# Kernel tuning notes

Measured on AMD Instinct MI355X. Metric: run time of the kernel, lower is better.

Reference implementation:

```python
import jax, jax.numpy as jnp
import numpy as np

N_NODES = 50000


def gcn_conv(x, src, dst, W, b, n_nodes):
    """PyG GCNConv: self-loops + symmetric normalization D^-1/2 (A+I) D^-1/2 X W + b."""
    loop = jnp.arange(n_nodes, dtype=src.dtype)
    s = jnp.concatenate([src, loop])
    d = jnp.concatenate([dst, loop])
    deg = jax.ops.segment_sum(jnp.ones_like(d, dtype=x.dtype), d, num_segments=n_nodes)
    dinv = jnp.where(deg > 0, jax.lax.rsqrt(deg), 0.0)
    norm = dinv[s] * dinv[d]  # (E+N,)
    h = x @ W  # (N, out)
    msg = h[s] * norm[:, None]
    return jax.ops.segment_sum(msg, d, num_segments=n_nodes) + b


def setup_inputs() -> dict:
    key = jax.random.key(0)
    ks = jax.random.split(key, 16)
    N, S, D = N_NODES, 20, 128
    E = 1_600_000
    PH, PO, GH, GO = 64, 128, 128, 32

    def lin(k, fan_in, fan_out):
        bound = 1.0 / np.sqrt(fan_in)
        kw, kb = jax.random.split(k)
        W = jax.random.uniform(kw, (fan_in, fan_out), jnp.float32, -bound, bound)
        b = jax.random.uniform(kb, (fan_out,), jnp.float32, -bound, bound)
        return W, b

    W_embed, b_embed = lin(ks[0], D, PH)
    W_attn, b_attn = lin(ks[1], PH, 1)
    W_out, b_out = lin(ks[2], PH, PO)
    W1, b1 = lin(ks[3], PO, GH)
    W2, b2 = lin(ks[4], GH, GO)
    Wm1, bm1 = lin(ks[5], GO, 64)
    Wm2, bm2 = lin(ks[6], 64, 1)

    return {
        "set_features": jax.random.normal(ks[7], (N, S, D), jnp.float32),
        "set_mask": jnp.ones((N, S), jnp.int32),
        "edge_index": jax.random.randint(ks[8], (2, E), 0, N, jnp.int32),
        "query_idx": jax.random.randint(ks[9], (4096,), 0, N, jnp.int32),
        "W_embed": W_embed, "b_embed": b_embed,
        "W_attn": W_attn, "b_attn": b_attn,
        "W_out": W_out, "b_out": b_out,
        "W1": W1, "b1": b1, "W2": W2, "b2": b2,
        "Wm1": Wm1, "bm1": bm1, "Wm2": Wm2, "bm2": bm2,
    }


def reference(set_features, set_mask, edge_index, query_idx,
              W_embed, b_embed, W_attn, b_attn, W_out, b_out,
              W1, b1, W2, b2, Wm1, bm1, Wm2, bm2):
    n_nodes = set_features.shape[0]
    # Attention pooling over each node's set: (N, S, D) -> (N, PO)
    z = jax.nn.relu(set_features @ W_embed + b_embed)          # (N, S, PH)
    scores = (z @ W_attn)[..., 0] + b_attn[0]                  # (N, S)
    scores = jnp.where(set_mask == 0, -jnp.inf, scores)
    attn = jax.nn.softmax(scores, axis=1)                      # (N, S)
    pooled = jnp.einsum('nsh,ns->nh', z, attn) @ W_out + b_out  # (N, PO)

    src, dst = edge_index[0], edge_index[1]
    x = jax.nn.relu(gcn_conv(pooled, src, dst, W1, b1, n_nodes))
    x = jax.nn.relu(gcn_conv(x, src, dst, W2, b2, n_nodes))

    q = x[query_idx]                                            # (B, GO)
    logits = (jax.nn.relu(q @ Wm1 + bm1) @ Wm2 + bm2)[..., 0]   # (B,)
    return logits
```

## Files before the change

### kernel.cpp

```cpp
#include <hip/hip_runtime.h>
#include <math.h>

#define RFL(x) __builtin_amdgcn_readfirstlane(x)
#define RL(x, l) __int_as_float(__builtin_amdgcn_readlane(__float_as_int(x), (l)))

typedef __attribute__((ext_vector_type(8))) short bf16x8;
typedef __attribute__((ext_vector_type(4))) float f32x4;

__device__ inline unsigned short bf16_rne(float f) {
  unsigned u = __float_as_uint(f);
  u += 0x7FFFu + ((u >> 16) & 1u);
  return (unsigned short)(u >> 16);
}


__global__ __launch_bounds__(256) void k_zero(int* p, int n) {
  int t = blockIdx.x * 256 + threadIdx.x;
  if (t < n) p[t] = 0;
}

__global__ __launch_bounds__(256) void k_count(const int* __restrict__ dst, int* cnt, int E) {
  int stride = gridDim.x * blockDim.x;
  for (int e = blockIdx.x * blockDim.x + threadIdx.x; e < E; e += stride)
    atomicAdd(&cnt[dst[e]], 1);
}


__global__ __launch_bounds__(256) void k_scan1(const int* __restrict__ cnt, int* __restrict__ row,
                                               int* __restrict__ partial, int N) {
  __shared__ int sm[256];
  int t = threadIdx.x, g = blockIdx.x * 256 + t;
  int v = (g < N) ? cnt[g] : 0;
  sm[t] = v;
  __syncthreads();
#pragma unroll
  for (int off = 1; off < 256; off <<= 1) {
    int x = 0;
    if (t >= off) x = sm[t - off];
    __syncthreads();
    if (t >= off) sm[t] += x;
    __syncthreads();
  }
  if (g < N) row[g] = sm[t] - v;
  if (t == 255) partial[blockIdx.x] = sm[255];
}

__global__ __launch_bounds__(256) void k_scan2(int* __restrict__ partial, int P) {
  __shared__ int sm[256];
  int t = threadIdx.x;
  int carry = 0;
  for (int base = 0; base < P; base += 256) {
    int idx = base + t;
    int v = (idx < P) ? partial[idx] : 0;
    sm[t] = v;
    __syncthreads();
#pragma unroll
    for (int off = 1; off < 256; off <<= 1) {
      int x = 0;
      if (t >= off) x = sm[t - off];
      __syncthreads();
      if (t >= off) sm[t] += x;
      __syncthreads();
    }
    if (idx < P) partial[idx] = carry + sm[t] - v;
    int tot = sm[255];
    __syncthreads();
    carry += tot;
  }
}

__global__ __launch_bounds__(256) void k_scan3(int* __restrict__ row, const int* __restrict__ partial,
                                               int* __restrict__ cursor, const int* __restrict__ cnt,
                                               float* __restrict__ dinv, int N) {
  int g = blockIdx.x * 256 + threadIdx.x;
  if (g < N) {
    int v = row[g] + partial[blockIdx.x];
    row[g] = v;
    cursor[g] = v;
    dinv[g] = rsqrtf((float)cnt[g] + 1.0f);
  }
}


__global__ __launch_bounds__(256) void k_edge_fill(const int* __restrict__ src, const int* __restrict__ dst,
                                                   int* __restrict__ cursor, int* __restrict__ esrc, int E) {
  int stride = gridDim.x * blockDim.x;
  for (int e = blockIdx.x * blockDim.x + threadIdx.x; e < E; e += stride) {
    int s = src[e], d = dst[e];
    int pos = atomicAdd(&cursor[d], 1);
    esrc[pos] = s;
  }
}


__global__ __launch_bounds__(256) void k_wc(const float* __restrict__ Wout, const float* __restrict__ bout,
                                            const float* __restrict__ W1, float* __restrict__ Wc,
                                            float* __restrict__ bc) {
  int t = blockIdx.x * 256 + threadIdx.x;
  if (t >= 65 * 128) return;
  int h = t >> 7, o = t & 127;
  const float* row = (h < 64) ? (Wout + h * 128) : bout;
  float a = 0.f;
  for (int d = 0; d < 128; ++d) a += row[d] * W1[d * 128 + o];
  if (h < 64) Wc[h * 128 + o] = a;
  else bc[o] = a;
}


__global__ __launch_bounds__(256, 3) void k_pool(const float* __restrict__ X, const int* __restrict__ mask,
                                                 const float* __restrict__ WE, const float* __restrict__ bE,
                                                 const float* __restrict__ WA, const float* __restrict__ bA,
                                                 const float* __restrict__ dinv, float* __restrict__ pzp, int N) {
  __shared__ __align__(16) unsigned short Xh[80][136];
  __shared__ __align__(16) unsigned short Xl[80][136];
  __shared__ float scorep[80][4];
  __shared__ float sco[80];
  __shared__ float wgtA[80];
  float* zt = (float*)&Xh[0][0];

  const int t = threadIdx.x;
  const int lane = t & 63;
  const int wv = t >> 6;
  const int cb = wv * 16;
  const int l16 = lane & 15;
  const int lg = lane >> 4;

  const long long totRows = (long long)N * 20;
  const int numTiles = (N + 3) / 4;

  const int r0 = t >> 5;
  const int kq4 = (t & 31) * 4;

  bf16x8 bh[4], bl[4];
#pragma unroll
  for (int kk = 0; kk < 4; ++kk) {
    union { bf16x8 v; unsigned short s[8]; } uh, ul;
#pragma unroll
    for (int i = 0; i < 8; ++i) {
      int k = kk * 32 + lg * 8 + i;
      float w = WE[k * 64 + cb + l16];
      unsigned short h = bf16_rne(w);
      uh.s[i] = h;
      ul.s[i] = bf16_rne(w - __uint_as_float((unsigned)h << 16));
    }
    bh[kk] = uh.v;
    bl[kk] = ul.v;
  }
  const float bEv = bE[cb + l16];
  const float WAv = WA[cb + l16];
  const float bAv = bA[0];
  const float NEG = -3.0e38f;

  int tile = blockIdx.x;
  if (tile >= numTiles) return;

  float4 xv[10];
#pragma unroll
  for (int q = 0; q < 10; ++q) {
    long long rr = (long long)tile * 80 + r0 + q * 8;
    if (rr >= totRows) rr = totRows - 1;
    xv[q] = *(const float4*)(X + rr * 128 + kq4);
  }
  int mkcur = 1;
  {
    long long mi = (long long)tile * 80 + t;
    if (t < 80) mkcur = (mi < totRows) ? mask[mi] : 0;
  }

  while (true) {
#pragma unroll
    for (int q = 0; q < 10; ++q) {
      const int r = r0 + q * 8;
      const float4 v = xv[q];
      unsigned short h0 = bf16_rne(v.x), h1 = bf16_rne(v.y), h2 = bf16_rne(v.z), h3 = bf16_rne(v.w);
      float f0 = __uint_as_float((unsigned)h0 << 16);
      float f1 = __uint_as_float((unsigned)h1 << 16);
      float f2 = __uint_as_float((unsigned)h2 << 16);
      float f3 = __uint_as_float((unsigned)h3 << 16);
      *(ushort4*)&Xh[r][kq4] = make_ushort4(h0, h1, h2, h3);
      *(ushort4*)&Xl[r][kq4] = make_ushort4(bf16_rne(v.x - f0), bf16_rne(v.y - f1),
                                            bf16_rne(v.z - f2), bf16_rne(v.w - f3));
    }
    __syncthreads();

    const int nextTile = tile + gridDim.x;
    const bool hasNext = nextTile < numTiles;
    float4 xn[10];
    int mknext = 1;
    {
      const long long nb = (long long)(hasNext ? nextTile : tile) * 80;
#pragma unroll
      for (int q = 0; q < 10; ++q) {
        long long rr = nb + r0 + q * 8;
        if (rr >= totRows) rr = totRows - 1;
        xn[q] = *(const float4*)(X + rr * 128 + kq4);
      }
      long long mi = nb + t;
      if (t < 80) mknext = (mi < totRows) ? mask[mi] : 0;
    }

    f32x4 acc[5];
#pragma unroll
    for (int rt = 0; rt < 5; ++rt) acc[rt] = (f32x4){0.f, 0.f, 0.f, 0.f};
#pragma unroll
    for (int rt = 0; rt < 5; ++rt) {
      const int rl = rt * 16 + l16;
#pragma unroll
      for (int kk = 0; kk < 4; ++kk) {
        const int ko = kk * 32 + lg * 8;
        bf16x8 ah = *(const bf16x8*)&Xh[rl][ko];
        bf16x8 al = *(const bf16x8*)&Xl[rl][ko];
        acc[rt] = __builtin_amdgcn_mfma_f32_16x16x32_bf16(ah, bh[kk], acc[rt], 0, 0, 0);
        acc[rt] = __builtin_amdgcn_mfma_f32_16x16x32_bf16(ah, bl[kk], acc[rt], 0, 0, 0);
        acc[rt] = __builtin_amdgcn_mfma_f32_16x16x32_bf16(al, bh[kk], acc[rt], 0, 0, 0);
      }
    }

#pragma unroll
    for (int rt = 0; rt < 5; ++rt) {
#pragma unroll
      for (int j = 0; j < 4; ++j) {
        float z = fmaxf(acc[rt][j] + bEv, 0.f);
        acc[rt][j] = z;
        float v = z * WAv;
        v += __shfl_xor(v, 1, 64);
        v += __shfl_xor(v, 2, 64);
        v += __shfl_xor(v, 4, 64);
        v += __shfl_xor(v, 8, 64);
        if (l16 == 0) scorep[rt * 16 + lg * 4 + j][wv] = v;
      }
    }
    __syncthreads();

#pragma unroll
    for (int rt = 0; rt < 5; ++rt) {
#pragma unroll
      for (int j = 0; j < 4; ++j) {
        int row = rt * 16 + lg * 4 + j;
        zt[row * 68 + cb + l16] = acc[rt][j];
      }
    }
    if (t < 80) {
      float4 sp = *(const float4*)scorep[t];
      float sc = sp.x + sp.y + sp.z + sp.w + bAv;
      if (mkcur == 0) sc = NEG;
      sco[t] = sc;
    }
    __syncthreads();

    if (t < 80) {
      const int base = (t / 20) * 20;
      float mx = NEG;
#pragma unroll
      for (int i = 0; i < 20; ++i) mx = fmaxf(mx, sco[base + i]);
      float den = 0.f;
#pragma unroll
      for (int i = 0; i < 20; ++i) den += __expf(sco[base + i] - mx);
      wgtA[t] = __expf(sco[t] - mx) / den;
    }
    __syncthreads();

    {
      int n = t >> 6, col = t & 63;
      long long node = (long long)tile * 4 + n;
      if (node < N) {
        float s = 0.f;
#pragma unroll
        for (int i = 0; i < 20; ++i) s += zt[(n * 20 + i) * 68 + col] * wgtA[n * 20 + i];
        pzp[node * 64 + col] = s * dinv[node];
      }
    }

    if (!hasNext) break;
    __syncthreads();
#pragma unroll
    for (int q = 0; q < 10; ++q) xv[q] = xn[q];
    mkcur = mknext;
    tile = nextTile;
  }
}


__global__ __launch_bounds__(256) void k_gather1(const int* __restrict__ row, const int* __restrict__ cnt,
                                                 const int* __restrict__ esrc, const float* __restrict__ pzp,
                                                 const float* __restrict__ dinv, float* __restrict__ y,
                                                 float* __restrict__ gout, int N) {
  const int lane = threadIdx.x & 63;
  const int node = RFL(blockIdx.x * 4 + (threadIdx.x >> 6));
  if (node >= N) return;
  const int q = lane >> 4, f4 = lane & 15;
  const int rs = RFL(row[node]);
  const int ne = RFL(cnt[node]);
  const float di = dinv[node];
  const float4* __restrict__ hv = (const float4*)pzp;
  float a0 = 0.f, a1 = 0.f, a2 = 0.f, a3 = 0.f, ds = 0.f;
  int j = 0;
  for (; j + 16 <= ne; j += 16) {
    const int b = rs + j + q * 4;
    int s[4];
#pragma unroll
    for (int u = 0; u < 4; ++u) s[u] = esrc[b + u];
    float4 v[4];
#pragma unroll
    for (int u = 0; u < 4; ++u) v[u] = hv[(size_t)s[u] * 16 + f4];
#pragma unroll
    for (int u = 0; u < 4; ++u) {
      a0 += v[u].x; a1 += v[u].y; a2 += v[u].z; a3 += v[u].w;
      ds += dinv[s[u]];
    }
  }
  if (j < ne) {
    const int b = j + q * 4;
    int s[4];
    float m[4];
#pragma unroll
    for (int u = 0; u < 4; ++u) {
      int idx = b + u;
      int c = (idx < ne) ? idx : (ne - 1);
      s[u] = esrc[rs + c];
      m[u] = (idx < ne) ? 1.f : 0.f;
    }
    float4 v[4];
#pragma unroll
    for (int u = 0; u < 4; ++u) v[u] = hv[(size_t)s[u] * 16 + f4];
#pragma unroll
    for (int u = 0; u < 4; ++u) {
      a0 += v[u].x * m[u]; a1 += v[u].y * m[u]; a2 += v[u].z * m[u]; a3 += v[u].w * m[u];
      ds += dinv[s[u]] * m[u];
    }
  }
  a0 += __shfl_xor(a0, 16, 64); a0 += __shfl_xor(a0, 32, 64);
  a1 += __shfl_xor(a1, 16, 64); a1 += __shfl_xor(a1, 32, 64);
  a2 += __shfl_xor(a2, 16, 64); a2 += __shfl_xor(a2, 32, 64);
  a3 += __shfl_xor(a3, 16, 64); a3 += __shfl_xor(a3, 32, 64);
  ds += __shfl_xor(ds, 16, 64); ds += __shfl_xor(ds, 32, 64);
  if (lane < 16) {
    float4 sv = hv[(size_t)node * 16 + f4];
    float4 o;
    o.x = (a0 + sv.x * di) * di;
    o.y = (a1 + sv.y * di) * di;
    o.z = (a2 + sv.z * di) * di;
    o.w = (a3 + sv.w * di) * di;
    ((float4*)y)[(size_t)node * 16 + f4] = o;
    if (f4 == 0) gout[node] = di * (ds + di * di);
  }
}


__global__ __launch_bounds__(256, 2) void k_gemm1(const float* __restrict__ y, const float* __restrict__ gin,
                                                  const float* __restrict__ Wc, const float* __restrict__ bc,
                                                  float* __restrict__ x1, int N) {
  const int lane = threadIdx.x & 63;
  float w0[64], w1[64];
#pragma unroll
  for (int d = 0; d < 64; ++d) {
    w0[d] = Wc[d * 128 + lane];
    w1[d] = Wc[d * 128 + 64 + lane];
  }
  const float b0 = bc[lane], b1v = bc[64 + lane];
  const int nw = (gridDim.x * blockDim.x) >> 6;
  const int w_id = (blockIdx.x * blockDim.x + threadIdx.x) >> 6;
  for (int r = w_id; r < N; r += nw) {
    const float xv = y[(size_t)r * 64 + lane];
    const float gr = gin[r];
    const int xi = __float_as_int(xv);
    float p0 = 0.f, p1 = 0.f, p2 = 0.f, p3 = 0.f;
#pragma unroll
    for (int d0 = 0; d0 < 64; d0 += 2) {
      float a0 = RL((float&)xi, d0);
      float a1 = RL((float&)xi, d0 + 1);
      p0 += a0 * w0[d0];
      p1 += a0 * w1[d0];
      p2 += a1 * w0[d0 + 1];
      p3 += a1 * w1[d0 + 1];
    }
    size_t o = (size_t)r * 128 + lane;
    x1[o] = p0 + p2 + gr * b0;
    x1[o + 64] = p1 + p3 + gr * b1v;
  }
}


__global__ __launch_bounds__(256, 2) void k_gemm2(const float* __restrict__ x1, const float* __restrict__ b1,
                                                  const float* __restrict__ W2, const float* __restrict__ dinv,
                                                  float* __restrict__ h2p, int N) {
  const int lane = threadIdx.x & 63;
  const int col = lane & 31;
  float w[128];
#pragma unroll
  for (int d = 0; d < 128; ++d) w[d] = W2[d * 32 + col];
  const float bb0 = b1[lane], bb1 = b1[64 + lane];
  const int nw = (gridDim.x * blockDim.x) >> 6;
  const int w_id = (blockIdx.x * blockDim.x + threadIdx.x) >> 6;
  for (int r = w_id; r < N; r += nw) {
    float rx0 = fmaxf(x1[(size_t)r * 128 + lane] + bb0, 0.f);
    float rx1 = fmaxf(x1[(size_t)r * 128 + 64 + lane] + bb1, 0.f);
    const int xi0 = __float_as_int(rx0), xi1 = __float_as_int(rx1);
    float p0 = 0.f, p1 = 0.f, p2 = 0.f, p3 = 0.f;
#pragma unroll
    for (int d0 = 0; d0 < 64; d0 += 2) {
      float a0 = RL((float&)xi0, d0);
      float a1 = RL((float&)xi0, d0 + 1);
      float c0 = RL((float&)xi1, d0);
      float c1 = RL((float&)xi1, d0 + 1);
      p0 += a0 * w[d0];
      p1 += a1 * w[d0 + 1];
      p2 += c0 * w[64 + d0];
      p3 += c1 * w[64 + d0 + 1];
    }
    if (lane < 32) {
      float di = dinv[r];
      h2p[(size_t)r * 32 + col] = ((p0 + p1) + (p2 + p3)) * di;
    }
  }
}


__global__ __launch_bounds__(256) void k_gmlp(const int* __restrict__ qidx, const int* __restrict__ row,
                                              const int* __restrict__ cnt, const int* __restrict__ esrc,
                                              const float* __restrict__ h2p, const float* __restrict__ dinv,
                                              const float* __restrict__ b2, const float* __restrict__ Wm1,
                                              const float* __restrict__ bm1, const float* __restrict__ Wm2,
                                              const float* __restrict__ bm2, float* __restrict__ out, int B) {
  __shared__ float qs[4][32];
  const int lane = threadIdx.x & 63;
  const int wv = threadIdx.x >> 6;
  const int w = blockIdx.x * 4 + wv;
  const int wc = (w < B) ? w : (B - 1);
  const int node = RFL(qidx[wc]);

  const int q = lane >> 3, f4 = lane & 7;
  const int rs = RFL(row[node]);
  const int ne = RFL(cnt[node]);
  const float di = dinv[node];
  const float4* __restrict__ hv = (const float4*)h2p;
  float a0 = 0.f, a1 = 0.f, a2 = 0.f, a3 = 0.f;
  int j = 0;
  for (; j + 32 <= ne; j += 32) {
    const int b = rs + j + q * 4;
    int s[4];
#pragma unroll
    for (int u = 0; u < 4; ++u) s[u] = esrc[b + u];
    float4 v[4];
#pragma unroll
    for (int u = 0; u < 4; ++u) v[u] = hv[(size_t)s[u] * 8 + f4];
#pragma unroll
    for (int u = 0; u < 4; ++u) {
      a0 += v[u].x; a1 += v[u].y; a2 += v[u].z; a3 += v[u].w;
    }
  }
  if (j < ne) {
    const int b = j + q * 4;
    int s[4];
    float m[4];
#pragma unroll
    for (int u = 0; u < 4; ++u) {
      int idx = b + u;
      int c = (idx < ne) ? idx : (ne - 1);
      s[u] = esrc[rs + c];
      m[u] = (idx < ne) ? 1.f : 0.f;
    }
    float4 v[4];
#pragma unroll
    for (int u = 0; u < 4; ++u) v[u] = hv[(size_t)s[u] * 8 + f4];
#pragma unroll
    for (int u = 0; u < 4; ++u) {
      a0 += v[u].x * m[u]; a1 += v[u].y * m[u]; a2 += v[u].z * m[u]; a3 += v[u].w * m[u];
    }
  }
#pragma unroll
  for (int off = 8; off <= 32; off <<= 1) {
    a0 += __shfl_xor(a0, off, 64);
    a1 += __shfl_xor(a1, off, 64);
    a2 += __shfl_xor(a2, off, 64);
    a3 += __shfl_xor(a3, off, 64);
  }
  if (q == 0) {
    float4 sv = hv[(size_t)node * 8 + f4];
    qs[wv][f4 * 4 + 0] = fmaxf((a0 + sv.x * di) * di + b2[f4 * 4 + 0], 0.f);
    qs[wv][f4 * 4 + 1] = fmaxf((a1 + sv.y * di) * di + b2[f4 * 4 + 1], 0.f);
    qs[wv][f4 * 4 + 2] = fmaxf((a2 + sv.z * di) * di + b2[f4 * 4 + 2], 0.f);
    qs[wv][f4 * 4 + 3] = fmaxf((a3 + sv.w * di) * di + b2[f4 * 4 + 3], 0.f);
  }
  __syncthreads();

  float h = bm1[lane];
#pragma unroll
  for (int k = 0; k < 32; ++k) h += qs[wv][k] * Wm1[k * 64 + lane];
  float r = fmaxf(h, 0.f) * Wm2[lane];
#pragma unroll
  for (int off = 1; off < 64; off <<= 1) r += __shfl_xor(r, off, 64);
  if (lane == 0 && w < B) out[w] = r + bm2[0];
}


extern "C" void kernel_launch(void* const* d_in, const int* in_sizes, int n_in,
                              void* d_out, int out_size, void* d_ws, size_t ws_size,
                              hipStream_t stream) {
  const float* X    = (const float*)d_in[0];
  const int*   mask = (const int*)d_in[1];
  const int*   ei   = (const int*)d_in[2];
  const int*   qidx = (const int*)d_in[3];
  const float* WE   = (const float*)d_in[4];
  const float* bE   = (const float*)d_in[5];
  const float* WA   = (const float*)d_in[6];
  const float* bA   = (const float*)d_in[7];
  const float* Wout = (const float*)d_in[8];
  const float* bout = (const float*)d_in[9];
  const float* W1   = (const float*)d_in[10];
  const float* b1   = (const float*)d_in[11];
  const float* W2   = (const float*)d_in[12];
  const float* b2   = (const float*)d_in[13];
  const float* Wm1  = (const float*)d_in[14];
  const float* bm1  = (const float*)d_in[15];
  const float* Wm2  = (const float*)d_in[16];
  const float* bm2  = (const float*)d_in[17];

  const int N = in_sizes[1] / 20;
  const int E = in_sizes[2] / 2;
  const int B = in_sizes[3];
  const int* src  = ei;
  const int* dstp = ei + E;

  const size_t Na = ((size_t)N + 63) & ~(size_t)63;
  const size_t Ea = ((size_t)E + 63) & ~(size_t)63;
  const int P = (N + 255) / 256;
  const size_t Pa = ((size_t)P + 63) & ~(size_t)63;

  float* ws      = (float*)d_ws;
  float* dinv    = ws;
  int*   cnt     = (int*)(dinv + Na);
  int*   rowp    = cnt + Na;
  int*   cursor  = rowp + Na;
  int*   partial = cursor + Na;
  int*   esrc    = partial + Pa;
  float* Wc      = (float*)(esrc + Ea);
  float* bc      = Wc + 8192;
  float* gbuf    = bc + 128;
  float* pzp     = gbuf + Na;
  float* y       = pzp + (size_t)N * 64;
  float* x1      = y + (size_t)N * 64;
  float* h2p     = pzp;

  const int nb = (N + 255) / 256;
  const int nw4 = (N + 3) / 4;
  const int poolBlocks = ((N + 3) / 4 < 768) ? (N + 3) / 4 : 768;

  k_zero<<<nb, 256, 0, stream>>>(cnt, N);
  k_count<<<1024, 256, 0, stream>>>(dstp, cnt, E);
  k_scan1<<<P, 256, 0, stream>>>(cnt, rowp, partial, N);
  k_scan2<<<1, 256, 0, stream>>>(partial, P);
  k_scan3<<<P, 256, 0, stream>>>(rowp, partial, cursor, cnt, dinv, N);
  k_edge_fill<<<1024, 256, 0, stream>>>(src, dstp, cursor, esrc, E);
  k_wc<<<33, 256, 0, stream>>>(Wout, bout, W1, Wc, bc);
  k_pool<<<poolBlocks, 256, 0, stream>>>(X, mask, WE, bE, WA, bA, dinv, pzp, N);
  k_gather1<<<nw4, 256, 0, stream>>>(rowp, cnt, esrc, pzp, dinv, y, gbuf, N);
  k_gemm1<<<1024, 256, 0, stream>>>(y, gbuf, Wc, bc, x1, N);
  k_gemm2<<<1024, 256, 0, stream>>>(x1, b1, W2, dinv, h2p, N);
  k_gmlp<<<(B + 3) / 4, 256, 0, stream>>>(qidx, rowp, cnt, esrc, h2p, dinv, b2, Wm1, bm1, Wm2, bm2,
                                          (float*)d_out, B);
}
```

Baseline: 476.2 us.

## Fold edge fill and weight combine into pool kernel, drop scan2

Removes the single-block scan2 kernel; each scan3 block now reduces the preceding partial sums itself. Moves CSR edge fill and the Wout·W1 weight fold into the start of k_pool so they share one launch with the pooling work. The softmax weights are now computed inline per output thread, which removes one barrier and shared buffer but repeats the exp work. This cuts three launches and their serialization gaps, at the cost of redundant per-thread reductions and atomic-heavy edge filling placed inside a register-bounded kernel.

```diff
diff --git a/kernel.cpp b/kernel.cpp
--- a/kernel.cpp
+++ b/kernel.cpp
@@ -45,36 +45,24 @@
   if (t == 255) partial[blockIdx.x] = sm[255];
 }
 
-__global__ __launch_bounds__(256) void k_scan2(int* __restrict__ partial, int P) {
-  __shared__ int sm[256];
-  int t = threadIdx.x;
-  int carry = 0;
-  for (int base = 0; base < P; base += 256) {
-    int idx = base + t;
-    int v = (idx < P) ? partial[idx] : 0;
-    sm[t] = v;
-    __syncthreads();
-#pragma unroll
-    for (int off = 1; off < 256; off <<= 1) {
-      int x = 0;
-      if (t >= off) x = sm[t - off];
-      __syncthreads();
-      if (t >= off) sm[t] += x;
-      __syncthreads();
-    }
-    if (idx < P) partial[idx] = carry + sm[t] - v;
-    int tot = sm[255];
-    __syncthreads();
-    carry += tot;
-  }
-}
-
 __global__ __launch_bounds__(256) void k_scan3(int* __restrict__ row, const int* __restrict__ partial,
                                                int* __restrict__ cursor, const int* __restrict__ cnt,
                                                float* __restrict__ dinv, int N) {
-  int g = blockIdx.x * 256 + threadIdx.x;
+  __shared__ int red[256];
+  const int t = threadIdx.x;
+  int acc = 0;
+  for (int i = t; i < blockIdx.x; i += 256) acc += partial[i];
+  red[t] = acc;
+  __syncthreads();
+#pragma unroll
+  for (int off = 128; off > 0; off >>= 1) {
+    if (t < off) red[t] += red[t + off];
+    __syncthreads();
+  }
+  const int base = red[0];
+  int g = blockIdx.x * 256 + t;
   if (g < N) {
-    int v = row[g] + partial[blockIdx.x];
+    int v = row[g] + base;
     row[g] = v;
     cursor[g] = v;
     dinv[g] = rsqrtf((float)cnt[g] + 1.0f);
@@ -82,43 +70,43 @@
 }
 
 
-__global__ __launch_bounds__(256) void k_edge_fill(const int* __restrict__ src, const int* __restrict__ dst,
-                                                   int* __restrict__ cursor, int* __restrict__ esrc, int E) {
-  int stride = gridDim.x * blockDim.x;
-  for (int e = blockIdx.x * blockDim.x + threadIdx.x; e < E; e += stride) {
-    int s = src[e], d = dst[e];
-    int pos = atomicAdd(&cursor[d], 1);
-    esrc[pos] = s;
-  }
-}
-
-
-__global__ __launch_bounds__(256) void k_wc(const float* __restrict__ Wout, const float* __restrict__ bout,
-                                            const float* __restrict__ W1, float* __restrict__ Wc,
-                                            float* __restrict__ bc) {
-  int t = blockIdx.x * 256 + threadIdx.x;
-  if (t >= 65 * 128) return;
-  int h = t >> 7, o = t & 127;
-  const float* row = (h < 64) ? (Wout + h * 128) : bout;
-  float a = 0.f;
-  for (int d = 0; d < 128; ++d) a += row[d] * W1[d * 128 + o];
-  if (h < 64) Wc[h * 128 + o] = a;
-  else bc[o] = a;
-}
-
-
 __global__ __launch_bounds__(256, 3) void k_pool(const float* __restrict__ X, const int* __restrict__ mask,
                                                  const float* __restrict__ WE, const float* __restrict__ bE,
                                                  const float* __restrict__ WA, const float* __restrict__ bA,
-                                                 const float* __restrict__ dinv, float* __restrict__ pzp, int N) {
+                                                 const float* __restrict__ dinv, float* __restrict__ pzp,
+                                                 const int* __restrict__ src, const int* __restrict__ dst,
+                                                 int* __restrict__ cursor, int* __restrict__ esrc, int E,
+                                                 const float* __restrict__ Wout, const float* __restrict__ bout,
+                                                 const float* __restrict__ W1, float* __restrict__ Wc,
+                                                 float* __restrict__ bc, int N) {
   __shared__ __align__(16) unsigned short Xh[80][136];
   __shared__ __align__(16) unsigned short Xl[80][136];
   __shared__ float scorep[80][4];
   __shared__ float sco[80];
-  __shared__ float wgtA[80];
   float* zt = (float*)&Xh[0][0];
 
   const int t = threadIdx.x;
+
+  {
+    const long long stride = (long long)gridDim.x * 256;
+    for (long long e = (long long)blockIdx.x * 256 + t; e < E; e += stride) {
+      int s = src[e], d = dst[e];
+      int pos = atomicAdd(&cursor[d], 1);
+      esrc[pos] = s;
+    }
+  }
+  if (blockIdx.x < 33) {
+    int tt = blockIdx.x * 256 + t;
+    if (tt < 65 * 128) {
+      int h = tt >> 7, o = tt & 127;
+      const float* rw = (h < 64) ? (Wout + h * 128) : bout;
+      float a = 0.f;
+      for (int d = 0; d < 128; ++d) a += rw[d] * W1[d * 128 + o];
+      if (h < 64) Wc[h * 128 + o] = a;
+      else bc[o] = a;
+    }
+  }
+
   const int lane = t & 63;
   const int wv = t >> 6;
   const int cb = wv * 16;
@@ -248,26 +236,21 @@
     }
     __syncthreads();
 
-    if (t < 80) {
-      const int base = (t / 20) * 20;
-      float mx = NEG;
-#pragma unroll
-      for (int i = 0; i < 20; ++i) mx = fmaxf(mx, sco[base + i]);
-      float den = 0.f;
-#pragma unroll
-      for (int i = 0; i < 20; ++i) den += __expf(sco[base + i] - mx);
-      wgtA[t] = __expf(sco[t] - mx) / den;
-    }
-    __syncthreads();
-
     {
       int n = t >> 6, col = t & 63;
       long long node = (long long)tile * 4 + n;
       if (node < N) {
+        const int base = n * 20;
+        float mx = NEG;
+#pragma unroll
+        for (int i = 0; i < 20; ++i) mx = fmaxf(mx, sco[base + i]);
+        float den = 0.f;
+#pragma unroll
+        for (int i = 0; i < 20; ++i) den += __expf(sco[base + i] - mx);
         float s = 0.f;
 #pragma unroll
-        for (int i = 0; i < 20; ++i) s += zt[(n * 20 + i) * 68 + col] * wgtA[n * 20 + i];
-        pzp[node * 64 + col] = s * dinv[node];
+        for (int i = 0; i < 20; ++i) s += zt[(base + i) * 68 + col] * __expf(sco[base + i] - mx);
+        pzp[node * 64 + col] = s / den * dinv[node];
       }
     }
 
@@ -549,11 +532,10 @@
   k_zero<<<nb, 256, 0, stream>>>(cnt, N);
   k_count<<<1024, 256, 0, stream>>>(dstp, cnt, E);
   k_scan1<<<P, 256, 0, stream>>>(cnt, rowp, partial, N);
-  k_scan2<<<1, 256, 0, stream>>>(partial, P);
   k_scan3<<<P, 256, 0, stream>>>(rowp, partial, cursor, cnt, dinv, N);
-  k_edge_fill<<<1024, 256, 0, stream>>>(src, dstp, cursor, esrc, E);
-  k_wc<<<33, 256, 0, stream>>>(Wout, bout, W1, Wc, bc);
-  k_pool<<<poolBlocks, 256, 0, stream>>>(X, mask, WE, bE, WA, bA, dinv, pzp, N);
+  k_pool<<<poolBlocks, 256, 0, stream>>>(X, mask, WE, bE, WA, bA, dinv, pzp,
+                                         src, dstp, cursor, esrc, E,
+                                         Wout, bout, W1, Wc, bc, N);
   k_gather1<<<nw4, 256, 0, stream>>>(rowp, cnt, esrc, pzp, dinv, y, gbuf, N);
   k_gemm1<<<1024, 256, 0, stream>>>(y, gbuf, Wc, bc, x1, N);
   k_gemm2<<<1024, 256, 0, stream>>>(x1, b1, W2, dinv, h2p, N);
```

Result: slower. 508.6 us (+6.8%).
